# Kernel optimization log

Hardware: AMD Instinct MI355X
Metric: run time of the kernel (lower is better)

## Reference

```python
import jax, jax.numpy as jnp
import numpy as np

N = 50000      # n_nodes
E = 800000     # n_edges (avg degree 16)
D_IN, D_HID, D_OUT = 128, 128, 64


def setup_inputs() -> dict:
    key = jax.random.key(0)
    k1, k2, k3, k4 = jax.random.split(key, 4)
    x = jax.random.normal(k1, (N, D_IN), jnp.float32)
    edge_index = jax.random.randint(k2, (2, E), 0, N, jnp.int32)
    # Glorot-style init for the two GCNConv linear weights
    W1 = jax.random.normal(k3, (D_IN, D_HID), jnp.float32) / np.sqrt(D_IN)
    W2 = jax.random.normal(k4, (D_HID, D_OUT), jnp.float32) / np.sqrt(D_HID)
    b1 = jnp.zeros((D_HID,), jnp.float32)
    b2 = jnp.zeros((D_OUT,), jnp.float32)
    return {"x": x, "edge_index": edge_index, "W1": W1, "b1": b1, "W2": W2, "b2": b2}


def _gcn_conv(x, W, b, src, dst):
    """PyG GCNConv: linear transform, then sym-normalized aggregation with self-loops."""
    h = x @ W                                   # [N, F_out]
    ones = jnp.ones((src.shape[0],), h.dtype)
    # degree includes the self-loop weight of 1
    deg = jax.ops.segment_sum(ones, dst, num_segments=N) + 1.0
    dinv = jax.lax.rsqrt(deg)                   # D^{-1/2}
    norm = dinv[src] * dinv[dst]                # per-edge normalization
    agg = jax.ops.segment_sum(h[src] * norm[:, None], dst, num_segments=N)
    # self-loop contribution: norm_ii = dinv_i^2
    return agg + h * (dinv * dinv)[:, None] + b


def reference(x, edge_index, W1, b1, W2, b2):
    src, dst = edge_index[0], edge_index[1]
    h = jax.nn.relu(_gcn_conv(x, W1, b1, src, dst))
    out = jax.nn.relu(_gcn_conv(h, W2, b2, src, dst))
    return out
```

## Files before the change

### kernel.cpp

```cpp
#include <hip/hip_runtime.h>

typedef unsigned short u16;
typedef __attribute__((ext_vector_type(8))) short short8;
typedef __attribute__((ext_vector_type(4))) float f32x4;

__device__ __forceinline__ float bf2f(u16 h) {
    union { unsigned u; float f; } v; v.u = ((unsigned)h) << 16; return v.f;
}
__device__ __forceinline__ float bflo(unsigned u) {
    union { unsigned u; float f; } v; v.u = u << 16; return v.f;
}
__device__ __forceinline__ float bfhi(unsigned u) {
    union { unsigned u; float f; } v; v.u = u & 0xFFFF0000u; return v.f;
}
__device__ __forceinline__ u16 f2bf(float f) {
    union { float f; unsigned u; } v; v.f = f;
    unsigned u = v.u;
    u += 0x7FFFu + ((u >> 16) & 1u);
    return (u16)(u >> 16);
}

__global__ void k_detect(const u16* __restrict__ x, int* __restrict__ flag) {
    __shared__ int c_s;
    if (threadIdx.x == 0) c_s = 0;
    __syncthreads();
    int c = 0;
    for (int i = threadIdx.x; i < 2048; i += blockDim.x) {
        int e = (x[2 * i] >> 7) & 0xFF;
        c += (e >= 160 || e <= 80) ? 1 : 0;
    }
    atomicAdd(&c_s, c);
    __syncthreads();
    if (threadIdx.x == 0) *flag = (c_s > 64) ? 1 : 0;
}

__global__ void k_convert(const void* __restrict__ in, u16* __restrict__ out,
                          int n, const int* __restrict__ flag) {
    int i = blockIdx.x * blockDim.x + threadIdx.x;
    if (i >= n) return;
    if (*flag) out[i] = f2bf(((const float*)in)[i]);
    else       out[i] = ((const u16*)in)[i];
}

__global__ void k_convert_w(const void* __restrict__ W1, const void* __restrict__ b1,
                            const void* __restrict__ W2, const void* __restrict__ b2,
                            u16* __restrict__ out, const int* __restrict__ flag) {
    const int n1 = 128 * 128, n2 = n1 + 128, n3 = n2 + 128 * 64, n4 = n3 + 64;
    int i = blockIdx.x * 256 + threadIdx.x;
    if (i >= n4) return;
    const void* src; int off;
    if (i < n1)      { src = W1; off = i; }
    else if (i < n2) { src = b1; off = i - n1; }
    else if (i < n3) { src = W2; off = i - n2; }
    else             { src = b2; off = i - n3; }
    out[i] = *flag ? f2bf(((const float*)src)[off]) : ((const u16*)src)[off];
}


__global__ void k_degree(const int* __restrict__ dst, int* __restrict__ cnt, int E) {
    int e = blockIdx.x * blockDim.x + threadIdx.x;
    if (e < E) atomicAdd(&cnt[dst[e]], 1);
}

__global__ void k_scan_blocks(const int* __restrict__ cnt, int* __restrict__ rowp,
                              int* __restrict__ sums, int n) {
    __shared__ int s[256];
    int t = threadIdx.x;
    int i = blockIdx.x * 256 + t;
    int v = (i < n) ? cnt[i] : 0;
    s[t] = v;
    __syncthreads();
    for (int off = 1; off < 256; off <<= 1) {
        int add = (t >= off) ? s[t - off] : 0;
        __syncthreads();
        s[t] += add;
        __syncthreads();
    }
    if (i < n) rowp[i] = s[t] - v;
    if (t == 255) sums[blockIdx.x] = s[255];
}

__global__ void k_scan_top(int* __restrict__ sums, int nb) {
    __shared__ int s[256];
    int t = threadIdx.x;
    int v = (t < nb) ? sums[t] : 0;
    s[t] = v;
    __syncthreads();
    for (int off = 1; off < 256; off <<= 1) {
        int add = (t >= off) ? s[t - off] : 0;
        __syncthreads();
        s[t] += add;
        __syncthreads();
    }
    sums[t] = s[t] - v;
}

__global__ void k_finalize(int* __restrict__ rowp, const int* __restrict__ sums,
                           const int* __restrict__ cnt, float* __restrict__ dinv,
                           int n, int E) {
    int i = blockIdx.x * 256 + threadIdx.x;
    if (i < n) {
        rowp[i] += sums[i >> 8];
        dinv[i] = rsqrtf((float)cnt[i] + 1.0f);
    }
    if (i == 0) rowp[n] = E;
}

__global__ void k_fill(const int* __restrict__ src, const int* __restrict__ dst,
                       const int* __restrict__ rowp, int* __restrict__ fill,
                       int* __restrict__ col, int E) {
    int e = blockIdx.x * blockDim.x + threadIdx.x;
    if (e < E) {
        int d = dst[e];
        int p = rowp[d] + atomicAdd(&fill[d], 1);
        col[p] = src[e];
    }
}


template <int NOUT>
__global__ void k_gemm_scale(const u16* __restrict__ A, const u16* __restrict__ W,
                             const float* __restrict__ dinv, u16* __restrict__ out, int M) {
    __shared__ u16 Wt[NOUT][136];
    int t = threadIdx.x;
    for (int idx = t; idx < NOUT * 128; idx += 256) {
        int k = idx / NOUT, n = idx % NOUT;
        Wt[n][k] = W[idx];
    }
    __syncthreads();
    int wave = t >> 6, lane = t & 63;
    int m0 = (blockIdx.x * 4 + wave) * 16;
    if (m0 >= M) return;
    int q = lane >> 4;
    int mr = lane & 15;

    const u16* arow = A + (size_t)(m0 + mr) * 128 + q * 8;
    short8 a[4];
#pragma unroll
    for (int c = 0; c < 4; c++) a[c] = *(const short8*)(arow + c * 32);

    f32x4 acc[NOUT / 16];
#pragma unroll
    for (int tl = 0; tl < NOUT / 16; tl++) acc[tl] = (f32x4){0.f, 0.f, 0.f, 0.f};

#pragma unroll
    for (int c = 0; c < 4; c++) {
#pragma unroll
        for (int tl = 0; tl < NOUT / 16; tl++) {
            short8 b = *(const short8*)(&Wt[tl * 16 + mr][c * 32 + q * 8]);
            acc[tl] = __builtin_amdgcn_mfma_f32_16x16x32_bf16(a[c], b, acc[tl], 0, 0, 0);
        }
    }

    int rbase = m0 + q * 4;
#pragma unroll
    for (int tl = 0; tl < NOUT / 16; tl++) {
#pragma unroll
        for (int r = 0; r < 4; r++) {
            int row = rbase + r;
            float v = acc[tl][r] * dinv[row];
            out[(size_t)row * NOUT + tl * 16 + mr] = f2bf(v);
        }
    }
}


template <int F>
__global__ void k_agg(const u16* __restrict__ g, const int* __restrict__ rowp,
                      const int* __restrict__ col, const float* __restrict__ dinv,
                      const u16* __restrict__ bias, u16* __restrict__ outh,
                      float* __restrict__ outf, const int* __restrict__ flag,
                      int N, int E) {
    constexpr int LPR = F / 8;
    constexpr int EPW = 64 / LPR;
    int d = blockIdx.x * 4 + (threadIdx.x >> 6);
    if (d >= N) return;
    int lane = threadIdx.x & 63;
    int er = lane / LPR;
    int fo = (lane % LPR) * 8;

    int beg = rowp[d], end = rowp[d + 1];
    if (beg < 0) beg = 0;
    if (end > E) end = E;
    int deg = end - beg;

    float a0[8], a1[8];
#pragma unroll
    for (int j = 0; j < 8; j++) { a0[j] = 0.f; a1[j] = 0.f; }

    for (int base = 0; base < deg; base += 64) {
        int cnt = deg - base; if (cnt > 64) cnt = 64;
        int colv = 0;
        if (lane < cnt) {
            int s = col[beg + base + lane];
            colv = s < 0 ? 0 : (s >= N ? N - 1 : s);
        }
        int full = cnt / EPW;
        int i = 0;
        for (; i + 2 <= full; i += 2) {
            int s0 = __shfl(colv, i * EPW + er, 64);
            int s1 = __shfl(colv, (i + 1) * EPW + er, 64);
            uint4 v0 = *(const uint4*)(g + (size_t)s0 * F + fo);
            uint4 v1 = *(const uint4*)(g + (size_t)s1 * F + fo);
            a0[0] += bflo(v0.x); a0[1] += bfhi(v0.x);
            a0[2] += bflo(v0.y); a0[3] += bfhi(v0.y);
            a0[4] += bflo(v0.z); a0[5] += bfhi(v0.z);
            a0[6] += bflo(v0.w); a0[7] += bfhi(v0.w);
            a1[0] += bflo(v1.x); a1[1] += bfhi(v1.x);
            a1[2] += bflo(v1.y); a1[3] += bfhi(v1.y);
            a1[4] += bflo(v1.z); a1[5] += bfhi(v1.z);
            a1[6] += bflo(v1.w); a1[7] += bfhi(v1.w);
        }
        if (i < full) {
            int s0 = __shfl(colv, i * EPW + er, 64);
            uint4 v0 = *(const uint4*)(g + (size_t)s0 * F + fo);
            a0[0] += bflo(v0.x); a0[1] += bfhi(v0.x);
            a0[2] += bflo(v0.y); a0[3] += bfhi(v0.y);
            a0[4] += bflo(v0.z); a0[5] += bfhi(v0.z);
            a0[6] += bflo(v0.w); a0[7] += bfhi(v0.w);
            i++;
        }
        int rem = cnt - full * EPW;
        int s0 = __shfl(colv, (full * EPW + er) & 63, 64);
        if (er < rem) {
            uint4 v0 = *(const uint4*)(g + (size_t)s0 * F + fo);
            a0[0] += bflo(v0.x); a0[1] += bfhi(v0.x);
            a0[2] += bflo(v0.y); a0[3] += bfhi(v0.y);
            a0[4] += bflo(v0.z); a0[5] += bfhi(v0.z);
            a0[6] += bflo(v0.w); a0[7] += bfhi(v0.w);
        }
    }
#pragma unroll
    for (int j = 0; j < 8; j++) a0[j] += a1[j];
#pragma unroll
    for (int off = LPR; off < 64; off <<= 1) {
#pragma unroll
        for (int j = 0; j < 8; j++) a0[j] += __shfl_xor(a0[j], off, 64);
    }

    if (lane < LPR) {
        uint4 sv = *(const uint4*)(g + (size_t)d * F + fo);
        uint4 bv = *(const uint4*)(bias + fo);
        float di = dinv[d];
        float r[8];
        r[0] = di * (a0[0] + bflo(sv.x)) + bflo(bv.x);
        r[1] = di * (a0[1] + bfhi(sv.x)) + bfhi(bv.x);
        r[2] = di * (a0[2] + bflo(sv.y)) + bflo(bv.y);
        r[3] = di * (a0[3] + bfhi(sv.y)) + bfhi(bv.y);
        r[4] = di * (a0[4] + bflo(sv.z)) + bflo(bv.z);
        r[5] = di * (a0[5] + bfhi(sv.z)) + bfhi(bv.z);
        r[6] = di * (a0[6] + bflo(sv.w)) + bflo(bv.w);
        r[7] = di * (a0[7] + bfhi(sv.w)) + bfhi(bv.w);
#pragma unroll
        for (int j = 0; j < 8; j++) r[j] = r[j] > 0.f ? r[j] : 0.f;
        size_t o = (size_t)d * F + fo;
        if (flag && *flag) {
            f32x4 w0 = {r[0], r[1], r[2], r[3]};
            f32x4 w1 = {r[4], r[5], r[6], r[7]};
            *(f32x4*)(outf + o) = w0;
            *(f32x4*)(outf + o + 4) = w1;
        } else {
            uint4 w;
            w.x = (unsigned)f2bf(r[0]) | ((unsigned)f2bf(r[1]) << 16);
            w.y = (unsigned)f2bf(r[2]) | ((unsigned)f2bf(r[3]) << 16);
            w.z = (unsigned)f2bf(r[4]) | ((unsigned)f2bf(r[5]) << 16);
            w.w = (unsigned)f2bf(r[6]) | ((unsigned)f2bf(r[7]) << 16);
            *(uint4*)(outh + o) = w;
        }
    }
}


extern "C" void kernel_launch(void* const* d_in, const int* in_sizes, int n_in,
                              void* d_out, int out_size, void* d_ws, size_t ws_size,
                              hipStream_t stream) {
    const int N = in_sizes[0] / 128;
    const int E = in_sizes[1] / 2;
    const int* ei = (const int*)d_in[1];
    const int* src = ei;
    const int* dst = ei + E;

    char* p = (char*)d_ws;
    auto alloc = [&](size_t b) { char* r = p; p += (b + 255) & ~(size_t)255; return r; };
    int*   flag = (int*)alloc(256);
    int*   rowp = (int*)alloc((size_t)(N + 1) * 4);
    float* dinv = (float*)alloc((size_t)N * 4);
    int*   col  = (int*)alloc((size_t)E * 4);
    u16*   wbuf = (u16*)alloc((size_t)(128 * 128 + 128 + 128 * 64 + 64) * 2);
    char*  slotA = alloc((size_t)N * 128 * 2);
    char*  slotB = alloc((size_t)N * 128 * 2);

    int* cnt  = (int*)slotA;
    int* fill = (int*)(slotA + (size_t)N * 4);
    int* sums = (int*)(slotA + (size_t)2 * N * 4);
    u16* g1   = (u16*)slotA;
    u16* g2   = (u16*)slotA;
    u16* xC   = (u16*)slotB;
    u16* o1   = (u16*)slotB;
    u16* W1C = wbuf;
    u16* b1C = wbuf + 128 * 128;
    u16* W2C = b1C + 128;
    u16* b2C = W2C + 128 * 64;

    k_detect<<<1, 256, 0, stream>>>((const u16*)d_in[0], flag);
    int xel = N * 128;
    k_convert<<<(xel + 255) / 256, 256, 0, stream>>>(d_in[0], xC, xel, flag);
    k_convert_w<<<97, 256, 0, stream>>>(d_in[2], d_in[3], d_in[4], d_in[5], wbuf, flag);

    hipMemsetAsync(slotA, 0, (size_t)2 * N * 4 + 1024, stream);
    int eb = (E + 255) / 256;
    int nb = (N + 255) / 256;
    k_degree<<<eb, 256, 0, stream>>>(dst, cnt, E);
    k_scan_blocks<<<nb, 256, 0, stream>>>(cnt, rowp, sums, N);
    k_scan_top<<<1, 256, 0, stream>>>(sums, nb);
    k_finalize<<<nb, 256, 0, stream>>>(rowp, sums, cnt, dinv, N, E);
    k_fill<<<eb, 256, 0, stream>>>(src, dst, rowp, fill, col, E);

    int gb = (N / 16 + 3) / 4;
    int ab = (N + 3) / 4;
    k_gemm_scale<128><<<gb, 256, 0, stream>>>(xC, W1C, dinv, g1, N);
    k_agg<128><<<ab, 256, 0, stream>>>(g1, rowp, col, dinv, b1C,
                                       o1, nullptr, nullptr, N, E);
    k_gemm_scale<64><<<gb, 256, 0, stream>>>(o1, W2C, dinv, g2, N);
    k_agg<64><<<ab, 256, 0, stream>>>(g2, rowp, col, dinv, b2C,
                                      (u16*)d_out, (float*)d_out, flag, N, E);
}
```

Before: 260.2 us.

## Fuse x conversion into first GEMM and record edge positions during degree count

Drops the standalone x conversion kernel: the first GEMM now reads fp32 or bf16 input directly based on the detect flag and converts to bf16 in registers. The degree kernel now stores each edge's atomic slot index, so the CSR fill kernel needs no second atomic pass or fill counter buffer. This removes one full pass over x (write plus reread) and one round of atomics over E edges, at the cost of an extra E-sized position buffer and wider fp32 loads in the GEMM.

```diff
diff --git a/kernel.cpp b/kernel.cpp
--- a/kernel.cpp
+++ b/kernel.cpp
@@ -32,14 +32,6 @@
     atomicAdd(&c_s, c);
     __syncthreads();
     if (threadIdx.x == 0) *flag = (c_s > 64) ? 1 : 0;
-}
-
-__global__ void k_convert(const void* __restrict__ in, u16* __restrict__ out,
-                          int n, const int* __restrict__ flag) {
-    int i = blockIdx.x * blockDim.x + threadIdx.x;
-    if (i >= n) return;
-    if (*flag) out[i] = f2bf(((const float*)in)[i]);
-    else       out[i] = ((const u16*)in)[i];
 }
 
 __global__ void k_convert_w(const void* __restrict__ W1, const void* __restrict__ b1,
@@ -57,9 +49,10 @@
 }
 
 
-__global__ void k_degree(const int* __restrict__ dst, int* __restrict__ cnt, int E) {
+__global__ void k_degpos(const int* __restrict__ dst, int* __restrict__ cnt,
+                         int* __restrict__ pos, int E) {
     int e = blockIdx.x * blockDim.x + threadIdx.x;
-    if (e < E) atomicAdd(&cnt[dst[e]], 1);
+    if (e < E) pos[e] = atomicAdd(&cnt[dst[e]], 1);
 }
 
 __global__ void k_scan_blocks(const int* __restrict__ cnt, int* __restrict__ rowp,
@@ -106,21 +99,18 @@
     if (i == 0) rowp[n] = E;
 }
 
-__global__ void k_fill(const int* __restrict__ src, const int* __restrict__ dst,
-                       const int* __restrict__ rowp, int* __restrict__ fill,
-                       int* __restrict__ col, int E) {
+__global__ void k_fill2(const int* __restrict__ src, const int* __restrict__ dst,
+                        const int* __restrict__ pos, const int* __restrict__ rowp,
+                        int* __restrict__ col, int E) {
     int e = blockIdx.x * blockDim.x + threadIdx.x;
-    if (e < E) {
-        int d = dst[e];
-        int p = rowp[d] + atomicAdd(&fill[d], 1);
-        col[p] = src[e];
-    }
+    if (e < E) col[rowp[dst[e]] + pos[e]] = src[e];
 }
 
 
 template <int NOUT>
-__global__ void k_gemm_scale(const u16* __restrict__ A, const u16* __restrict__ W,
-                             const float* __restrict__ dinv, u16* __restrict__ out, int M) {
+__global__ void k_gemm_scale(const void* __restrict__ Av, const u16* __restrict__ W,
+                             const float* __restrict__ dinv, u16* __restrict__ out,
+                             int M, const int* __restrict__ flag) {
     __shared__ u16 Wt[NOUT][136];
     int t = threadIdx.x;
     for (int idx = t; idx < NOUT * 128; idx += 256) {
@@ -134,10 +124,23 @@
     int q = lane >> 4;
     int mr = lane & 15;
 
-    const u16* arow = A + (size_t)(m0 + mr) * 128 + q * 8;
     short8 a[4];
-#pragma unroll
-    for (int c = 0; c < 4; c++) a[c] = *(const short8*)(arow + c * 32);
+    if (flag && *flag) {
+        const float* arow = (const float*)Av + (size_t)(m0 + mr) * 128 + q * 8;
+#pragma unroll
+        for (int c = 0; c < 4; c++) {
+            f32x4 lo = *(const f32x4*)(arow + c * 32);
+            f32x4 hi = *(const f32x4*)(arow + c * 32 + 4);
+            a[c][0] = (short)f2bf(lo.x); a[c][1] = (short)f2bf(lo.y);
+            a[c][2] = (short)f2bf(lo.z); a[c][3] = (short)f2bf(lo.w);
+            a[c][4] = (short)f2bf(hi.x); a[c][5] = (short)f2bf(hi.y);
+            a[c][6] = (short)f2bf(hi.z); a[c][7] = (short)f2bf(hi.w);
+        }
+    } else {
+        const u16* arow = (const u16*)Av + (size_t)(m0 + mr) * 128 + q * 8;
+#pragma unroll
+        for (int c = 0; c < 4; c++) a[c] = *(const short8*)(arow + c * 32);
+    }
 
     f32x4 acc[NOUT / 16];
 #pragma unroll
@@ -291,11 +294,10 @@
     char*  slotB = alloc((size_t)N * 128 * 2);
 
     int* cnt  = (int*)slotA;
-    int* fill = (int*)(slotA + (size_t)N * 4);
-    int* sums = (int*)(slotA + (size_t)2 * N * 4);
+    int* sums = (int*)(slotA + (size_t)N * 4);
     u16* g1   = (u16*)slotA;
     u16* g2   = (u16*)slotA;
-    u16* xC   = (u16*)slotB;
+    int* pos  = (int*)slotB;
     u16* o1   = (u16*)slotB;
     u16* W1C = wbuf;
     u16* b1C = wbuf + 128 * 128;
@@ -303,25 +305,23 @@
     u16* b2C = W2C + 128 * 64;
 
     k_detect<<<1, 256, 0, stream>>>((const u16*)d_in[0], flag);
-    int xel = N * 128;
-    k_convert<<<(xel + 255) / 256, 256, 0, stream>>>(d_in[0], xC, xel, flag);
     k_convert_w<<<97, 256, 0, stream>>>(d_in[2], d_in[3], d_in[4], d_in[5], wbuf, flag);
 
-    hipMemsetAsync(slotA, 0, (size_t)2 * N * 4 + 1024, stream);
+    hipMemsetAsync(slotA, 0, (size_t)N * 4 + 1024, stream);
     int eb = (E + 255) / 256;
     int nb = (N + 255) / 256;
-    k_degree<<<eb, 256, 0, stream>>>(dst, cnt, E);
+    k_degpos<<<eb, 256, 0, stream>>>(dst, cnt, pos, E);
     k_scan_blocks<<<nb, 256, 0, stream>>>(cnt, rowp, sums, N);
     k_scan_top<<<1, 256, 0, stream>>>(sums, nb);
     k_finalize<<<nb, 256, 0, stream>>>(rowp, sums, cnt, dinv, N, E);
-    k_fill<<<eb, 256, 0, stream>>>(src, dst, rowp, fill, col, E);
+    k_fill2<<<eb, 256, 0, stream>>>(src, dst, pos, rowp, col, E);
 
     int gb = (N / 16 + 3) / 4;
     int ab = (N + 3) / 4;
-    k_gemm_scale<128><<<gb, 256, 0, stream>>>(xC, W1C, dinv, g1, N);
+    k_gemm_scale<128><<<gb, 256, 0, stream>>>(d_in[0], W1C, dinv, g1, N, flag);
     k_agg<128><<<ab, 256, 0, stream>>>(g1, rowp, col, dinv, b1C,
                                        o1, nullptr, nullptr, N, E);
-    k_gemm_scale<64><<<gb, 256, 0, stream>>>(o1, W2C, dinv, g2, N);
+    k_gemm_scale<64><<<gb, 256, 0, stream>>>(o1, W2C, dinv, g2, N, nullptr);
     k_agg<64><<<ab, 256, 0, stream>>>(g2, rowp, col, dinv, b2C,
                                       (u16*)d_out, (float*)d_out, flag, N, E);
 }
```

New measurement: 218.7 us. 16.0% less time.
